# Optimization experiments

Hardware: AMD Instinct MI355X
Metric: run time of the kernel (lower is better)

The kernel has to match this reference:

```python
import jax, jax.numpy as jnp
import numpy as np

B, N, D, H = 4, 1024, 512, 8
DH = D // H  # per-head dim for V and for each of the two Q/K halves
LAM = 0.5


def setup_inputs() -> dict:
    key = jax.random.key(0)
    ks = jax.random.split(key, 7)
    s = 0.02
    return {
        "x": jax.random.normal(ks[0], (B, N, D), dtype=jnp.float32),
        "Wq": jax.random.normal(ks[1], (D, 2 * D), dtype=jnp.float32) * s,
        "bq": jax.random.normal(ks[2], (2 * D,), dtype=jnp.float32) * s,
        "Wk": jax.random.normal(ks[3], (D, 2 * D), dtype=jnp.float32) * s,
        "bk": jax.random.normal(ks[4], (2 * D,), dtype=jnp.float32) * s,
        "Wv": jax.random.normal(ks[5], (D, D), dtype=jnp.float32) * s,
        "bv": jax.random.normal(ks[6], (D,), dtype=jnp.float32) * s,
    }


def reference(x, Wq, bq, Wk, bk, Wv, bv):
    b, n, d = x.shape
    q = (x @ Wq + bq).reshape(b, n, H, 2 * DH).transpose(0, 2, 1, 3)  # [B,H,N,2*DH]
    k = (x @ Wk + bk).reshape(b, n, H, 2 * DH).transpose(0, 2, 1, 3)
    v = (x @ Wv + bv).reshape(b, n, H, DH).transpose(0, 2, 1, 3)      # [B,H,N,DH]
    q1, q2 = q[..., :DH], q[..., DH:]
    k1, k2 = k[..., :DH], k[..., DH:]
    scale = 1.0 / jnp.sqrt(jnp.float32(DH))
    a1 = jax.nn.softmax(jnp.einsum("bhqd,bhkd->bhqk", q1, k1) * scale, axis=-1)
    a2 = jax.nn.softmax(jnp.einsum("bhqd,bhkd->bhqk", q2, k2) * scale, axis=-1)
    attn = a1 - LAM * a2                                              # [B,H,N,N]
    out = jnp.einsum("bhqk,bhkd->bhqd", attn, v)                      # [B,H,N,DH]
    return out.transpose(0, 2, 1, 3).reshape(b, n, d)
```

## Files before the change

kernel.cpp:

```cpp
#include <hip/hip_runtime.h>
#include <hip/hip_bf16.h>

typedef unsigned short u16;
typedef unsigned int u32;
typedef short s16x8 __attribute__((ext_vector_type(8)));
typedef short s16x4 __attribute__((ext_vector_type(4)));
typedef float f32x4 __attribute__((ext_vector_type(4)));
typedef float f32x16 __attribute__((ext_vector_type(16)));

__device__ inline u16 f2bf(float f) {
  union { float f; unsigned int u; } v; v.f = f;
  unsigned int r = v.u + 0x7fffu + ((v.u >> 16) & 1u);
  return (u16)(r >> 16);
}

__device__ __forceinline__ u32 cvt_pk_bf16(float lo, float hi) {
  u32 r;
  asm("v_cvt_pk_bf16_f32 %0, %1, %2" : "=v"(r) : "v"(lo), "v"(hi));
  return r;
}

__device__ __forceinline__ void g2lds16(const u16* g, u16* l) {
  __builtin_amdgcn_global_load_lds((const __attribute__((address_space(1))) void*)g,
                                   (__attribute__((address_space(3))) void*)l, 16, 0, 0);
}

__global__ __launch_bounds__(256) void prep_kernel(const float* __restrict__ x, u16* __restrict__ xb,
                                                   const float* __restrict__ Wq,
                                                   const float* __restrict__ Wk,
                                                   const float* __restrict__ Wv,
                                                   u16* __restrict__ wt) {
  if (blockIdx.x >= 40) {
    int i = (((blockIdx.x - 40) * 8 + blockIdx.y) * 256 + threadIdx.x) * 8;
    float4 a = *(const float4*)(x + i);
    float4 b = *(const float4*)(x + i + 4);
    s16x8 o;
    o[0] = (short)f2bf(a.x); o[1] = (short)f2bf(a.y);
    o[2] = (short)f2bf(a.z); o[3] = (short)f2bf(a.w);
    o[4] = (short)f2bf(b.x); o[5] = (short)f2bf(b.y);
    o[6] = (short)f2bf(b.z); o[7] = (short)f2bf(b.w);
    *(s16x8*)(xb + i) = o;
    return;
  }
  __shared__ float tile[64][65];
  int jg = blockIdx.x * 64;
  const float* src; int C, j0;
  if (jg < 1024)      { src = Wq; C = 1024; j0 = jg; }
  else if (jg < 2048) { src = Wk; C = 1024; j0 = jg - 1024; }
  else                { src = Wv; C = 512;  j0 = jg - 2048; }
  int k0 = blockIdx.y * 64;
  int tx = threadIdx.x % 64, ty4 = threadIdx.x / 64;
#pragma unroll
  for (int p = 0; p < 16; ++p) {
    int r = p * 4 + ty4;
    tile[r][tx] = src[(size_t)(k0 + r) * C + j0 + tx];
  }
  __syncthreads();
#pragma unroll
  for (int p = 0; p < 16; ++p) {
    int r = p * 4 + ty4;
    wt[(size_t)(jg + r) * 512 + k0 + tx] = f2bf(tile[tx][r]);
  }
}

__global__ __launch_bounds__(256, 2) void gemm_qkv(const u16* __restrict__ xb, const u16* __restrict__ wt,
                                                   const float* __restrict__ bq, const float* __restrict__ bk,
                                                   const float* __restrict__ bv,
                                                   u16* __restrict__ qa, u16* __restrict__ ka,
                                                   u16* __restrict__ va) {
  __shared__ __align__(16) u16 As[128 * 64];
  __shared__ __align__(16) u16 Bs[128 * 64];
  int m0 = blockIdx.x * 128, j0 = blockIdx.y * 128;
  bool isV = (j0 >= 2048);
  int tid = threadIdx.x;
  int w = tid >> 6, lane = tid & 63, quad = lane >> 4, l16 = lane & 15;
  int wr = (w >> 1) * 64, wc = (w & 1) * 64;

  int srow[4], scol[4], sbase[4];
#pragma unroll
  for (int it = 0; it < 4; ++it) {
    int s = it * 256 + tid;
    srow[it] = s >> 3;
    scol[it] = (s & 7) ^ ((s >> 3) & 7);
    sbase[it] = (s & ~63) * 8;
  }

  f32x4 acc[4][4];
#pragma unroll
  for (int i = 0; i < 4; ++i)
#pragma unroll
    for (int j = 0; j < 4; ++j)
#pragma unroll
      for (int r = 0; r < 4; ++r) acc[i][j][r] = 0.f;

  for (int kk = 0; kk < 8; ++kk) {
    int k0 = kk * 64;
    __syncthreads();
#pragma unroll
    for (int it = 0; it < 4; ++it) {
      g2lds16(xb + (size_t)(m0 + srow[it]) * 512 + k0 + scol[it] * 8, &As[sbase[it]]);
      g2lds16(wt + (size_t)(j0 + srow[it]) * 512 + k0 + scol[it] * 8, &Bs[sbase[it]]);
    }
    __syncthreads();
#pragma unroll
    for (int kb = 0; kb < 2; ++kb) {
      s16x8 af[4], bfr[4];
#pragma unroll
      for (int rb = 0; rb < 4; ++rb) {
        int row = wr + rb * 16 + l16;
        af[rb] = *(const s16x8*)(&As[row * 64 + (((kb * 4 + quad) ^ (row & 7)) * 8)]);
      }
#pragma unroll
      for (int cb = 0; cb < 4; ++cb) {
        int row = wc + cb * 16 + l16;
        bfr[cb] = *(const s16x8*)(&Bs[row * 64 + (((kb * 4 + quad) ^ (row & 7)) * 8)]);
      }
      if (isV) {
#pragma unroll
        for (int rb = 0; rb < 4; ++rb)
#pragma unroll
          for (int cb = 0; cb < 4; ++cb)
            acc[rb][cb] = __builtin_amdgcn_mfma_f32_16x16x32_bf16(bfr[cb], af[rb], acc[rb][cb], 0, 0, 0);
      } else {
#pragma unroll
        for (int rb = 0; rb < 4; ++rb)
#pragma unroll
          for (int cb = 0; cb < 4; ++cb)
            acc[rb][cb] = __builtin_amdgcn_mfma_f32_16x16x32_bf16(af[rb], bfr[cb], acc[rb][cb], 0, 0, 0);
      }
    }
  }

  if (isV) {
#pragma unroll
    for (int cb = 0; cb < 4; ++cb) {
#pragma unroll
      for (int rb = 0; rb < 4; ++rb) {
        int m = m0 + wr + rb * 16 + l16;
        int bidx = m >> 10, n = m & 1023;
#pragma unroll
        for (int r = 0; r < 4; ++r) {
          int jj = j0 - 2048 + wc + cb * 16 + quad * 4 + r;
          int h = jj >> 6, d = jj & 63;
          float bias = bv[jj];
          va[((size_t)((bidx * 8 + h) * 64 + d)) * 1024 + n] = f2bf(acc[rb][cb][r] + bias);
        }
      }
    }
  } else {
#pragma unroll
    for (int cb = 0; cb < 4; ++cb) {
      int j = j0 + wc + cb * 16 + l16;
      bool isQ = (j < 1024);
      float bias = isQ ? bq[j] : bk[j - 1024];
#pragma unroll
      for (int rb = 0; rb < 4; ++rb) {
#pragma unroll
        for (int r = 0; r < 4; ++r) {
          int m = m0 + wr + rb * 16 + quad * 4 + r;
          int bidx = m >> 10, n = m & 1023;
          float val = acc[rb][cb][r] + bias;
          u16 o = f2bf(isQ ? val * 0.18033688f : val);
          if (isQ) {
            int h = j >> 7, r2 = j & 127;
            qa[((size_t)((bidx * 8 + h) * 1024 + n)) * 128 + r2] = o;
          } else {
            int jj = j - 1024, h = jj >> 7, r2 = jj & 127;
            ka[((size_t)((bidx * 8 + h) * 1024 + n)) * 128 + r2] = o;
          }
        }
      }
    }
  }
}

__global__ __launch_bounds__(256, 2) void attn_kernel(const u16* __restrict__ qa, const u16* __restrict__ ka,
                                                      const u16* __restrict__ va, float* __restrict__ out) {
  __shared__ __align__(16) u16 smem[24576];
  int bh = blockIdx.x, b = bh >> 3, h = bh & 7;
  int q0 = blockIdx.y * 64;
  int tid = threadIdx.x, w = tid >> 6, lane = tid & 63;
  int l32 = lane & 31, hi = lane >> 5;
  int team = w >> 1, wq = w & 1, t = tid & 127;
  u16* hb = smem + team * 12288;
  u16* const KbA = hb;
  u16* const KbB = hb + 4096;
  u16* const VbA = hb + 8192;
  u16* const VbB = hb + 10240;

  const u16* qrow = qa + (size_t)(bh * 1024 + q0 + wq * 32 + l32) * 128;
  s16x8 qf[2][4];
#pragma unroll
  for (int hh = 0; hh < 2; ++hh)
#pragma unroll
    for (int kb = 0; kb < 4; ++kb)
      qf[hh][kb] = *(const s16x8*)(qrow + 64 * hh + 16 * kb + 8 * hi);

  f32x16 O1[2], O2[2];
#pragma unroll
  for (int d = 0; d < 2; ++d)
#pragma unroll
    for (int r = 0; r < 16; ++r) { O1[d][r] = 0.f; O2[d][r] = 0.f; }
  float ds1 = 0.f, ds2 = 0.f;

  int r0 = t >> 4, c0 = t & 15;
  int rv = t >> 2, cv = (t & 3) ^ ((t >> 3) & 3);
  const u16* kgbase = ka + (size_t)bh * 1024 * 128;
  const u16* vgbase = va + (size_t)bh * 64 * 1024;
  int nbase = team * 512;

  auto stageK = [&](int n0, u16* Kd) {
#pragma unroll
    for (int it = 0; it < 4; ++it) {
      int row = it * 8 + r0;
      g2lds16(kgbase + (size_t)(n0 + row) * 128 + (c0 ^ (row & 15)) * 8,
              Kd + (it * 128 + (t & 64)) * 8);
    }
  };
  auto stageV = [&](int n0, u16* Vd) {
#pragma unroll
    for (int it = 0; it < 2; ++it) {
      int row = it * 32 + rv;
      g2lds16(vgbase + (size_t)row * 1024 + n0 + cv * 8,
              Vd + (it * 128 + (t & 64)) * 8);
    }
  };

  stageK(nbase, KbA);
  stageV(nbase, VbA);
  __syncthreads();

  for (int kt = 0; kt < 16; ++kt) {
    int cur = kt & 1;
    u16* const KsC = cur ? KbB : KbA;
    u16* const VsC = cur ? VbB : VbA;
    if (kt < 15) {
      int n1 = nbase + (kt + 1) * 32;
      stageK(n1, cur ? KbA : KbB);
      stageV(n1, cur ? VbA : VbB);
    }

    s16x8 pa[2][2];
#pragma unroll
    for (int hh = 0; hh < 2; ++hh) {
      f32x16 sv;
#pragma unroll
      for (int r = 0; r < 16; ++r) sv[r] = 0.f;
      int rbase = l32 * 128, rx15 = l32 & 15;
#pragma unroll
      for (int kb = 0; kb < 4; ++kb) {
        s16x8 kf = *(const s16x8*)(&KsC[rbase + (((8 * hh + 2 * kb + hi) ^ rx15) * 8)]);
        sv = __builtin_amdgcn_mfma_f32_32x32x16_bf16(kf, qf[hh][kb], sv, 0, 0, 0);
      }
      float dsl = 0.f;
#pragma unroll
      for (int s = 0; s < 2; ++s) {
        float e[8];
#pragma unroll
        for (int j = 0; j < 8; ++j) {
          e[j] = __builtin_exp2f(sv[s * 8 + j]);
          dsl += e[j];
        }
        union { u32 wd[4]; s16x8 v; } u;
        u.wd[0] = cvt_pk_bf16(e[0], e[1]);
        u.wd[1] = cvt_pk_bf16(e[2], e[3]);
        u.wd[2] = cvt_pk_bf16(e[4], e[5]);
        u.wd[3] = cvt_pk_bf16(e[6], e[7]);
        pa[hh][s] = u.v;
      }
      if (hh == 0) ds1 += dsl; else ds2 += dsl;
    }

    s16x8 vB[2][2];
#pragma unroll
    for (int dblk = 0; dblk < 2; ++dblk) {
      int row = dblk * 32 + l32, rbase = row * 32, rx = (row >> 1) & 3;
#pragma unroll
      for (int s = 0; s < 2; ++s) {
        union { s16x4 hl[2]; s16x8 v; } u;
        u.hl[0] = *(const s16x4*)(&VsC[rbase + (((2 * s) ^ rx) * 8) + 4 * hi]);
        u.hl[1] = *(const s16x4*)(&VsC[rbase + (((2 * s + 1) ^ rx) * 8) + 4 * hi]);
        vB[s][dblk] = u.v;
      }
    }

#pragma unroll
    for (int s = 0; s < 2; ++s)
#pragma unroll
      for (int dblk = 0; dblk < 2; ++dblk) {
        O1[dblk] = __builtin_amdgcn_mfma_f32_32x32x16_bf16(pa[0][s], vB[s][dblk], O1[dblk], 0, 0, 0);
        O2[dblk] = __builtin_amdgcn_mfma_f32_32x32x16_bf16(pa[1][s], vB[s][dblk], O2[dblk], 0, 0, 0);
      }

    __syncthreads();
  }

  float* scr = (float*)smem;
  int mbase = wq * 4224 + lane;
  if (team == 1) {
#pragma unroll
    for (int r = 0; r < 16; ++r) {
      scr[mbase + r * 64]        = O1[0][r];
      scr[mbase + (16 + r) * 64] = O1[1][r];
      scr[mbase + (32 + r) * 64] = O2[0][r];
      scr[mbase + (48 + r) * 64] = O2[1][r];
    }
    scr[mbase + 64 * 64] = ds1;
    scr[mbase + 65 * 64] = ds2;
  }
  __syncthreads();
  if (team == 0) {
#pragma unroll
    for (int r = 0; r < 16; ++r) {
      O1[0][r] += scr[mbase + r * 64];
      O1[1][r] += scr[mbase + (16 + r) * 64];
      O2[0][r] += scr[mbase + (32 + r) * 64];
      O2[1][r] += scr[mbase + (48 + r) * 64];
    }
    ds1 += scr[mbase + 64 * 64];
    ds2 += scr[mbase + 65 * 64];
    ds1 += __shfl_xor(ds1, 32, 64);
    ds2 += __shfl_xor(ds2, 32, 64);
    float inv1 = 1.0f / ds1, inv2 = 1.0f / ds2;
#pragma unroll
    for (int r = 0; r < 16; ++r) {
      int iq = (r & 3) + 8 * (r >> 2) + 4 * hi;
      float i1 = __shfl(inv1, iq, 64);
      float i2 = __shfl(inv2, iq, 64);
      size_t orow = (size_t)(b * 1024 + q0 + wq * 32 + iq) * 512 + h * 64 + l32;
      out[orow]      = O1[0][r] * i1 - 0.5f * O2[0][r] * i2;
      out[orow + 32] = O1[1][r] * i1 - 0.5f * O2[1][r] * i2;
    }
  }
}

extern "C" void kernel_launch(void* const* d_in, const int* in_sizes, int n_in,
                              void* d_out, int out_size, void* d_ws, size_t ws_size,
                              hipStream_t stream) {
  (void)in_sizes; (void)n_in; (void)out_size; (void)ws_size;
  const float* x  = (const float*)d_in[0];
  const float* Wq = (const float*)d_in[1];
  const float* bq = (const float*)d_in[2];
  const float* Wk = (const float*)d_in[3];
  const float* bk = (const float*)d_in[4];
  const float* Wv = (const float*)d_in[5];
  const float* bv = (const float*)d_in[6];
  float* out = (float*)d_out;

  char* ws = (char*)d_ws;
  u16* xb = (u16*)(ws);
  u16* wt = (u16*)(ws + 4194304);
  u16* qa = (u16*)(ws + 6815744);
  u16* ka = (u16*)(ws + 15204352);
  u16* va = (u16*)(ws + 23592960);

  prep_kernel<<<dim3(168, 8), 256, 0, stream>>>(x, xb, Wq, Wk, Wv, wt);
  gemm_qkv<<<dim3(32, 20), 256, 0, stream>>>(xb, wt, bq, bk, bv, qa, ka, va);
  attn_kernel<<<dim3(32, 16), 256, 0, stream>>>(qa, ka, va, out);
}
```

Baseline: 128.3 us.

## Double-buffer QKV GEMM LDS tiles with K=32 stages to overlap loads

```diff
diff --git a/kernel.cpp b/kernel.cpp
--- a/kernel.cpp
+++ b/kernel.cpp
@@ -68,21 +68,21 @@
                                                    const float* __restrict__ bv,
                                                    u16* __restrict__ qa, u16* __restrict__ ka,
                                                    u16* __restrict__ va) {
-  __shared__ __align__(16) u16 As[128 * 64];
-  __shared__ __align__(16) u16 Bs[128 * 64];
+  __shared__ __align__(16) u16 As[2][128 * 32];
+  __shared__ __align__(16) u16 Bs[2][128 * 32];
   int m0 = blockIdx.x * 128, j0 = blockIdx.y * 128;
   bool isV = (j0 >= 2048);
   int tid = threadIdx.x;
   int w = tid >> 6, lane = tid & 63, quad = lane >> 4, l16 = lane & 15;
   int wr = (w >> 1) * 64, wc = (w & 1) * 64;
 
-  int srow[4], scol[4], sbase[4];
-#pragma unroll
-  for (int it = 0; it < 4; ++it) {
+  int grow[2], gsrc[2], gdst[2];
+#pragma unroll
+  for (int it = 0; it < 2; ++it) {
     int s = it * 256 + tid;
-    srow[it] = s >> 3;
-    scol[it] = (s & 7) ^ ((s >> 3) & 7);
-    sbase[it] = (s & ~63) * 8;
+    grow[it] = s >> 2;
+    gsrc[it] = ((s & 3) ^ ((s >> 3) & 3)) * 8;
+    gdst[it] = (s & ~63) * 8;
   }
 
   f32x4 acc[4][4];
@@ -93,42 +93,48 @@
 #pragma unroll
       for (int r = 0; r < 4; ++r) acc[i][j][r] = 0.f;
 
-  for (int kk = 0; kk < 8; ++kk) {
-    int k0 = kk * 64;
+#pragma unroll
+  for (int it = 0; it < 2; ++it) {
+    g2lds16(xb + (size_t)(m0 + grow[it]) * 512 + gsrc[it], &As[0][gdst[it]]);
+    g2lds16(wt + (size_t)(j0 + grow[it]) * 512 + gsrc[it], &Bs[0][gdst[it]]);
+  }
+  __syncthreads();
+
+  for (int kt = 0; kt < 16; ++kt) {
+    int cur = kt & 1;
+    if (kt < 15) {
+      int k1 = (kt + 1) * 32;
+#pragma unroll
+      for (int it = 0; it < 2; ++it) {
+        g2lds16(xb + (size_t)(m0 + grow[it]) * 512 + k1 + gsrc[it], &As[cur ^ 1][gdst[it]]);
+        g2lds16(wt + (size_t)(j0 + grow[it]) * 512 + k1 + gsrc[it], &Bs[cur ^ 1][gdst[it]]);
+      }
+    }
+    s16x8 af[4], bfr[4];
+#pragma unroll
+    for (int rb = 0; rb < 4; ++rb) {
+      int row = wr + rb * 16 + l16;
+      af[rb] = *(const s16x8*)(&As[cur][row * 32 + ((quad ^ ((row >> 1) & 3)) * 8)]);
+    }
+#pragma unroll
+    for (int cb = 0; cb < 4; ++cb) {
+      int row = wc + cb * 16 + l16;
+      bfr[cb] = *(const s16x8*)(&Bs[cur][row * 32 + ((quad ^ ((row >> 1) & 3)) * 8)]);
+    }
+    if (isV) {
+#pragma unroll
+      for (int rb = 0; rb < 4; ++rb)
+#pragma unroll
+        for (int cb = 0; cb < 4; ++cb)
+          acc[rb][cb] = __builtin_amdgcn_mfma_f32_16x16x32_bf16(bfr[cb], af[rb], acc[rb][cb], 0, 0, 0);
+    } else {
+#pragma unroll
+      for (int rb = 0; rb < 4; ++rb)
+#pragma unroll
+        for (int cb = 0; cb < 4; ++cb)
+          acc[rb][cb] = __builtin_amdgcn_mfma_f32_16x16x32_bf16(af[rb], bfr[cb], acc[rb][cb], 0, 0, 0);
+    }
     __syncthreads();
-#pragma unroll
-    for (int it = 0; it < 4; ++it) {
-      g2lds16(xb + (size_t)(m0 + srow[it]) * 512 + k0 + scol[it] * 8, &As[sbase[it]]);
-      g2lds16(wt + (size_t)(j0 + srow[it]) * 512 + k0 + scol[it] * 8, &Bs[sbase[it]]);
-    }
-    __syncthreads();
-#pragma unroll
-    for (int kb = 0; kb < 2; ++kb) {
-      s16x8 af[4], bfr[4];
-#pragma unroll
-      for (int rb = 0; rb < 4; ++rb) {
-        int row = wr + rb * 16 + l16;
-        af[rb] = *(const s16x8*)(&As[row * 64 + (((kb * 4 + quad) ^ (row & 7)) * 8)]);
-      }
-#pragma unroll
-      for (int cb = 0; cb < 4; ++cb) {
-        int row = wc + cb * 16 + l16;
-        bfr[cb] = *(const s16x8*)(&Bs[row * 64 + (((kb * 4 + quad) ^ (row & 7)) * 8)]);
-      }
-      if (isV) {
-#pragma unroll
-        for (int rb = 0; rb < 4; ++rb)
-#pragma unroll
-          for (int cb = 0; cb < 4; ++cb)
-            acc[rb][cb] = __builtin_amdgcn_mfma_f32_16x16x32_bf16(bfr[cb], af[rb], acc[rb][cb], 0, 0, 0);
-      } else {
-#pragma unroll
-        for (int rb = 0; rb < 4; ++rb)
-#pragma unroll
-          for (int cb = 0; cb < 4; ++cb)
-            acc[rb][cb] = __builtin_amdgcn_mfma_f32_16x16x32_bf16(af[rb], bfr[cb], acc[rb][cb], 0, 0, 0);
-      }
-    }
   }
 
   if (isV) {
```

New measurement: 131.9 us. 1.03x slower.
